# Kernel tuning notes

Hardware: AMD Instinct MI355X
Metric: run time of the kernel (lower is better)

The kernel has to match this reference:

```python
import jax, jax.numpy as jnp
import numpy as np

TAU_THETA = 1.0   # membrane threshold V_th
GAMMA = 0.95      # spike reset decay factor
BETA = 0.95       # membrane leak factor

T, N = 128, 262144


def setup_inputs() -> dict:
    key = jax.random.key(0)
    I_in = jax.random.normal(key, (T, N), dtype=jnp.float32)
    return {"I_in": I_in}


def reference(I_in):
    # LIF recurrence over time via lax.scan (one fused sequential kernel).
    n = I_in.shape[1]
    v0 = jnp.zeros((n,), dtype=I_in.dtype)
    s0 = jnp.zeros((n,), dtype=I_in.dtype)

    def step(carry, I_t):
        v, s = carry
        v = BETA * v + I_t - GAMMA * s          # leak + input - reset current
        s = (v > TAU_THETA).astype(v.dtype)      # spike if above threshold
        v = v * (1.0 - s)                        # hard reset where spiked
        return (v, s), (s, v)

    _, (spikes, v_mem) = jax.lax.scan(step, (v0, s0), I_in)
    return (spikes, v_mem, spikes)
```

## Files before the change

### kernel.cpp

```cpp
#include <hip/hip_runtime.h>


#define T_STEPS 128
#define SPLIT 2
#define T_CHUNK (T_STEPS / SPLIT)
#define BETA_F 0.95f
#define GAMMA_F 0.95f
#define VTH_F 1.0f

typedef float f32x4 __attribute__((ext_vector_type(4)));

#define LIF_STEP(in)                                                            \
    do {                                                                        \
        vx = __fsub_rn(__fadd_rn(__fmul_rn(BETA_F, vx), (in).x), __fmul_rn(GAMMA_F, sx)); \
        vy = __fsub_rn(__fadd_rn(__fmul_rn(BETA_F, vy), (in).y), __fmul_rn(GAMMA_F, sy)); \
        vz = __fsub_rn(__fadd_rn(__fmul_rn(BETA_F, vz), (in).z), __fmul_rn(GAMMA_F, sz)); \
        vw = __fsub_rn(__fadd_rn(__fmul_rn(BETA_F, vw), (in).w), __fmul_rn(GAMMA_F, sw)); \
        sx = (vx > VTH_F) ? 1.0f : 0.0f;                                        \
        sy = (vy > VTH_F) ? 1.0f : 0.0f;                                        \
        sz = (vz > VTH_F) ? 1.0f : 0.0f;                                        \
        sw = (vw > VTH_F) ? 1.0f : 0.0f;                                        \
        vx = (sx != 0.0f) ? 0.0f : vx;                                          \
        vy = (sy != 0.0f) ? 0.0f : vy;                                          \
        vz = (sz != 0.0f) ? 0.0f : vz;                                          \
        vw = (sw != 0.0f) ? 0.0f : vw;                                          \
    } while (0)

__global__ __launch_bounds__(256) void lif_kernel(
    const f32x4* __restrict__ I4,
    f32x4* __restrict__ s_out,
    f32x4* __restrict__ v_out,
    f32x4* __restrict__ s_out2,
    int n4)
{
    const int nblk = gridDim.x / SPLIT;
    const int chunk = blockIdx.x / nblk;
    const int bcol = blockIdx.x % nblk;
    const int idx = bcol * blockDim.x + threadIdx.x;
    if (idx >= n4) return;

    float vx = 0.f, vy = 0.f, vz = 0.f, vw = 0.f;
    float sx = 0.f, sy = 0.f, sz = 0.f, sw = 0.f;

    size_t off = (size_t)idx;
    const int t0 = chunk * T_CHUNK;

    #pragma unroll 8
    for (int t = 0; t < t0; ++t, off += (size_t)n4) {
        f32x4 in = I4[off];
        LIF_STEP(in);
    }

    #pragma unroll 8
    for (int t = 0; t < T_CHUNK; ++t, off += (size_t)n4) {
        f32x4 in = I4[off];
        LIF_STEP(in);
        f32x4 sv; sv.x = sx; sv.y = sy; sv.z = sz; sv.w = sw;
        f32x4 vv; vv.x = vx; vv.y = vy; vv.z = vz; vv.w = vw;
        __builtin_nontemporal_store(sv, &s_out[off]);
        __builtin_nontemporal_store(vv, &v_out[off]);
        __builtin_nontemporal_store(sv, &s_out2[off]);
    }
}

extern "C" void kernel_launch(void* const* d_in, const int* in_sizes, int n_in,
                              void* d_out, int out_size, void* d_ws, size_t ws_size,
                              hipStream_t stream) {
    const float* I = (const float*)d_in[0];
    float* out = (float*)d_out;

    const int TN = in_sizes[0];
    const int N = TN / T_STEPS;
    const int n4 = N / 4;

    float* s0 = out;
    float* vm = out + (size_t)TN;
    float* s1 = out + 2 * (size_t)TN;

    const int block = 256;
    const int nblk = (n4 + block - 1) / block;
    const int grid = nblk * SPLIT;

    lif_kernel<<<grid, block, 0, stream>>>(
        (const f32x4*)I, (f32x4*)s0, (f32x4*)vm, (f32x4*)s1, n4);
}
```

Baseline: 80.53 us.

## Remove time-split recompute and software-pipeline input loads in register groups

```diff
diff --git a/kernel.cpp b/kernel.cpp
--- a/kernel.cpp
+++ b/kernel.cpp
@@ -2,8 +2,8 @@
 
 
 #define T_STEPS 128
-#define SPLIT 2
-#define T_CHUNK (T_STEPS / SPLIT)
+#define GROUP 8
+#define NGROUP (T_STEPS / GROUP)
 #define BETA_F 0.95f
 #define GAMMA_F 0.95f
 #define VTH_F 1.0f
@@ -33,33 +33,47 @@
     f32x4* __restrict__ s_out2,
     int n4)
 {
-    const int nblk = gridDim.x / SPLIT;
-    const int chunk = blockIdx.x / nblk;
-    const int bcol = blockIdx.x % nblk;
-    const int idx = bcol * blockDim.x + threadIdx.x;
+    const int idx = blockIdx.x * blockDim.x + threadIdx.x;
     if (idx >= n4) return;
 
     float vx = 0.f, vy = 0.f, vz = 0.f, vw = 0.f;
     float sx = 0.f, sy = 0.f, sz = 0.f, sw = 0.f;
 
-    size_t off = (size_t)idx;
-    const int t0 = chunk * T_CHUNK;
+    const size_t stride = (size_t)n4;
+    size_t loadOff  = (size_t)idx;
+    size_t storeOff = (size_t)idx;
 
-    #pragma unroll 8
-    for (int t = 0; t < t0; ++t, off += (size_t)n4) {
-        f32x4 in = I4[off];
-        LIF_STEP(in);
-    }
+    f32x4 buf[GROUP];
 
-    #pragma unroll 8
-    for (int t = 0; t < T_CHUNK; ++t, off += (size_t)n4) {
-        f32x4 in = I4[off];
-        LIF_STEP(in);
-        f32x4 sv; sv.x = sx; sv.y = sy; sv.z = sz; sv.w = sw;
-        f32x4 vv; vv.x = vx; vv.y = vy; vv.z = vz; vv.w = vw;
-        __builtin_nontemporal_store(sv, &s_out[off]);
-        __builtin_nontemporal_store(vv, &v_out[off]);
-        __builtin_nontemporal_store(sv, &s_out2[off]);
+    #pragma unroll
+    for (int j = 0; j < GROUP; ++j)
+        buf[j] = I4[loadOff + (size_t)j * stride];
+    loadOff += (size_t)GROUP * stride;
+
+    #pragma unroll
+    for (int g = 0; g < NGROUP; ++g) {
+        f32x4 nbuf[GROUP];
+        if (g + 1 < NGROUP) {
+            #pragma unroll
+            for (int j = 0; j < GROUP; ++j)
+                nbuf[j] = I4[loadOff + (size_t)j * stride];
+        }
+        loadOff += (size_t)GROUP * stride;
+
+        #pragma unroll
+        for (int j = 0; j < GROUP; ++j) {
+            LIF_STEP(buf[j]);
+            f32x4 sv; sv.x = sx; sv.y = sy; sv.z = sz; sv.w = sw;
+            f32x4 vv; vv.x = vx; vv.y = vy; vv.z = vz; vv.w = vw;
+            __builtin_nontemporal_store(sv, &s_out[storeOff]);
+            __builtin_nontemporal_store(vv, &v_out[storeOff]);
+            __builtin_nontemporal_store(sv, &s_out2[storeOff]);
+            storeOff += stride;
+        }
+
+        #pragma unroll
+        for (int j = 0; j < GROUP; ++j)
+            buf[j] = nbuf[j];
     }
 }
 
@@ -78,8 +92,7 @@
     float* s1 = out + 2 * (size_t)TN;
 
     const int block = 256;
-    const int nblk = (n4 + block - 1) / block;
-    const int grid = nblk * SPLIT;
+    const int grid = (n4 + block - 1) / block;
 
     lif_kernel<<<grid, block, 0, stream>>>(
         (const f32x4*)I, (f32x4*)s0, (f32x4*)vm, (f32x4*)s1, n4);
```

Result: faster. 75.62 us (-6.1%).
